# Kernel optimization log

Measured on AMD Instinct MI355X. Metric: run time of the kernel, lower is better.

## Reference

```python
import jax, jax.numpy as jnp
import numpy as np

B, S, D, H = 16, 577, 768, 12  # batch, seq (24*24+1 cls), hidden, heads
WH, WW = 24, 24
HEAD = D // H
NUM_REL = (2 * WH - 1) * (2 * WW - 1) + 3  # 2212


def make_rel_pos_index(wh, ww):
    # mirrors TFData2VecVisionRelativePositionBias.get_position_index
    xx, yy = np.meshgrid(np.arange(wh), np.arange(ww))  # 'xy' indexing like tf.meshgrid
    coords = np.stack([yy, xx], axis=0).reshape(2, -1)  # [2, wh*ww]
    rel = coords[:, :, None] - coords[:, None, :]       # [2, N, N]
    rel = rel.transpose(1, 2, 0)                        # [N, N, 2]
    rx = (rel[:, :, 0] + wh - 1) * (2 * ww - 1)
    ry = rel[:, :, 1] + ww - 1
    idx = rx + ry                                       # [N, N]
    n = idx.shape[0]
    top = np.full((1, n), NUM_REL - 3, dtype=idx.dtype)
    left = np.full((n, 1), NUM_REL - 2, dtype=idx.dtype)
    corner = np.full((1, 1), NUM_REL - 1, dtype=idx.dtype)
    idx = np.concatenate([top, idx], axis=0)
    idx = np.concatenate([np.concatenate([corner, left], axis=0), idx], axis=1)
    return idx.astype(np.int32)  # [N+1, N+1]


def setup_inputs() -> dict:
    key = jax.random.key(0)
    ks = jax.random.split(key, 6)
    scale = 0.02
    return {
        "hidden_states": jax.random.normal(ks[0], (B, S, D), jnp.float32),
        "Wq": jax.random.normal(ks[1], (D, D), jnp.float32) * scale,
        "bq": jnp.zeros((D,), jnp.float32),
        "Wk": jax.random.normal(ks[2], (D, D), jnp.float32) * scale,
        "Wv": jax.random.normal(ks[3], (D, D), jnp.float32) * scale,
        "bv": jnp.zeros((D,), jnp.float32),
        "rel_pos_bias_table": jax.random.normal(ks[4], (NUM_REL, H), jnp.float32) * scale,
        "rel_pos_index": jnp.asarray(make_rel_pos_index(WH, WW)),
    }


def reference(hidden_states, Wq, bq, Wk, Wv, bv, rel_pos_bias_table, rel_pos_index):
    b, s, _ = hidden_states.shape
    q = (hidden_states @ Wq + bq).reshape(b, s, H, HEAD).transpose(0, 2, 1, 3)
    k = (hidden_states @ Wk).reshape(b, s, H, HEAD).transpose(0, 2, 1, 3)
    v = (hidden_states @ Wv + bv).reshape(b, s, H, HEAD).transpose(0, 2, 1, 3)
    scores = jnp.einsum("bhqd,bhkd->bhqk", q, k) / jnp.sqrt(jnp.float32(HEAD))
    # gathered relative position bias: [S, S, H] -> [H, S, S]
    bias = rel_pos_bias_table[rel_pos_index].transpose(2, 0, 1)
    scores = scores + bias[None]
    probs = jax.nn.softmax(scores, axis=-1)
    out = jnp.einsum("bhqk,bhkd->bhqd", probs, v)
    out = out.transpose(0, 2, 1, 3).reshape(b, s, D)
    return out
```

## Files before the change

kernel.cpp:

```cpp
#include <hip/hip_runtime.h>
#include <hip/hip_bf16.h>


typedef __attribute__((ext_vector_type(8))) short bf16x8;
typedef __attribute__((ext_vector_type(4))) float f32x4;
typedef unsigned short u16;

#define SEQ 577
#define MTOT 9232
#define QKV_STRIDE 7090176
#define VT_PITCH 640
#define B_PITCH 640

static __device__ __forceinline__ u16 f2bf(float x) {
  unsigned int u = __float_as_uint(x);
  u = (u + 0x7FFFu + ((u >> 16) & 1u)) >> 16;
  return (u16)u;
}
static __device__ __forceinline__ float bf2f(u16 v) {
  return __uint_as_float(((unsigned int)v) << 16);
}

static __device__ __forceinline__ void gload_lds16(const void* g, void* l) {
  __builtin_amdgcn_global_load_lds(
      (const __attribute__((address_space(1))) unsigned int*)g,
      (__attribute__((address_space(3))) unsigned int*)l, 16, 0, 0);
}

__global__ __launch_bounds__(256) void prep(
    const float* __restrict__ Wq, const float* __restrict__ Wk,
    const float* __restrict__ Wv, const float* __restrict__ X,
    u16* __restrict__ WT, u16* __restrict__ Xb) {
  const int bid = blockIdx.x;
  if (bid < 1728) {
    __shared__ float t[32][33];
    const int z = bid / 576;
    const int rem = bid - z * 576;
    const int kx = rem % 24, ny = rem / 24;
    const float* W = (z == 0) ? Wq : (z == 1) ? Wk : Wv;
    int x = threadIdx.x & 31;
    int y = threadIdx.x >> 5;
    int k0 = kx * 32;
    int n0 = ny * 32;
#pragma unroll
    for (int i = 0; i < 4; ++i)
      t[y + i * 8][x] = W[(size_t)(k0 + y + i * 8) * 768 + n0 + x];
    __syncthreads();
    u16* o = WT + (size_t)z * 589824;
#pragma unroll
    for (int i = 0; i < 4; ++i)
      o[(size_t)(n0 + y + i * 8) * 768 + k0 + x] = f2bf(t[x][y + i * 8]);
  } else {
    size_t i = ((size_t)(bid - 1728) * 256 + threadIdx.x) * 8;
    if (i >= (size_t)MTOT * 768) return;
    const float4* xp = (const float4*)(X + i);
    float4 a = xp[0], b = xp[1];
    u16 pk[8] = {f2bf(a.x), f2bf(a.y), f2bf(a.z), f2bf(a.w),
                 f2bf(b.x), f2bf(b.y), f2bf(b.z), f2bf(b.w)};
    *(int4*)(Xb + i) = *(const int4*)pk;
  }
}

__global__ __launch_bounds__(256) void bias_pre(
    const float* __restrict__ table, const int* __restrict__ idx,
    u16* __restrict__ biasm) {
  int q = blockIdx.x;
  int h = blockIdx.y;
  for (int k = threadIdx.x; k < B_PITCH; k += 256) {
    u16 v = 0;
    if (k < SEQ) v = f2bf(table[idx[q * SEQ + k] * 12 + h]);
    biasm[((size_t)h * SEQ + q) * B_PITCH + k] = v;
  }
}

__global__ __launch_bounds__(256) void transpose_v(
    const u16* __restrict__ v,
    u16* __restrict__ vT) {
  const int tile = blockIdx.x;
  const int bh = blockIdx.y;
  const int b = bh / 12, h = bh % 12;
  const int tid = threadIdx.x;
  __shared__ u16 T[128][64];
  const int s0 = tile * 128;
  const u16* vp = v + (size_t)b * SEQ * 768 + h * 64;
#pragma unroll
  for (int it = 0; it < 4; ++it) {
    int c = tid + it * 256;
    int r = c >> 3, ko = (c & 7) << 3;
    int gs = s0 + r;
    int4 val = make_int4(0, 0, 0, 0);
    if (gs < SEQ) val = *(const int4*)(vp + (size_t)gs * 768 + ko);
    *(int4*)&T[r][ko ^ (((r >> 3) & 7) << 3)] = val;
  }
  __syncthreads();
  u16* op = vT + (size_t)bh * 64 * VT_PITCH;
#pragma unroll
  for (int it = 0; it < 4; ++it) {
    int c = tid + it * 256;
    int d = c >> 4, so = (c & 15) << 3;
    u16 tmp[8];
#pragma unroll
    for (int j = 0; j < 8; ++j) {
      int rr = so + j;
      tmp[j] = T[rr][d ^ (((rr >> 3) & 7) << 3)];
    }
    *(int4*)(op + (size_t)d * VT_PITCH + s0 + so) = *(const int4*)tmp;
  }
}

__global__ __launch_bounds__(256) void qkv_gemm(
    const u16* __restrict__ Xb,
    const u16* __restrict__ WT,
    const float* __restrict__ bq, const float* __restrict__ bv,
    u16* __restrict__ qkv) {
  const int bid = blockIdx.x;
  const int xcd = bid & 7;
  const int local = bid >> 3;
  const int mp = (local / 18) * 8 + xcd;
  if (mp >= 73) return;
  const int nw = local % 18;
  const int widx = nw % 3;
  const int m0 = mp * 128;
  const int n0 = (nw / 3) * 128;

  const int tid = threadIdx.x;
  const int lane = tid & 63;
  const int w = tid >> 6;
  const int wm = (w >> 1) * 64;
  const int wn = (w & 1) * 64;
  const int quad = lane >> 4;
  const int l15 = lane & 15;

  __shared__ u16 SH[2][128][32];

  const u16* Wp = WT + (size_t)widx * 589824;

  const int srow = w * 32 + (lane >> 2);
  const int scol = (lane & 3) * 8;

  f32x4 acc[4][4];
#pragma unroll
  for (int i = 0; i < 4; ++i)
#pragma unroll
    for (int j = 0; j < 4; ++j) acc[i][j] = (f32x4){0.f, 0.f, 0.f, 0.f};

  for (int kt = 0; kt < 24; ++kt) {
    const int k0 = kt * 32;
    {
      int r0 = m0 + srow;
      int r1 = r0 + 16;
      if (r0 > MTOT - 1) r0 = MTOT - 1;
      if (r1 > MTOT - 1) r1 = MTOT - 1;
      gload_lds16(Xb + (size_t)r0 * 768 + k0 + scol, &SH[0][w * 32][0]);
      gload_lds16(Xb + (size_t)r1 * 768 + k0 + scol, &SH[0][w * 32 + 16][0]);
      gload_lds16(Wp + (size_t)(n0 + srow) * 768 + k0 + scol, &SH[1][w * 32][0]);
      gload_lds16(Wp + (size_t)(n0 + srow + 16) * 768 + k0 + scol, &SH[1][w * 32 + 16][0]);
    }
    __syncthreads();
    bf16x8 af[4], bfv[4];
#pragma unroll
    for (int i = 0; i < 4; ++i)
      af[i] = *(const bf16x8*)(&SH[0][wm + i * 16 + l15][quad * 8]);
#pragma unroll
    for (int i = 0; i < 4; ++i)
      bfv[i] = *(const bf16x8*)(&SH[1][wn + i * 16 + l15][quad * 8]);
#pragma unroll
    for (int mt = 0; mt < 4; ++mt)
#pragma unroll
      for (int nt = 0; nt < 4; ++nt)
        acc[mt][nt] = __builtin_amdgcn_mfma_f32_16x16x32_bf16(af[mt], bfv[nt],
                                                              acc[mt][nt], 0, 0, 0);
    __syncthreads();
  }

  const float scale = (widx == 0) ? 0.125f : 1.0f;
  u16* ob = qkv + (size_t)widx * QKV_STRIDE;
  float biasv[4];
#pragma unroll
  for (int nt = 0; nt < 4; ++nt) {
    int n = n0 + wn + nt * 16 + l15;
    biasv[nt] = (widx == 0) ? bq[n] * 0.125f : (widx == 2) ? bv[n] : 0.f;
  }
  u16* S = &SH[0][0][0];
#pragma unroll
  for (int half = 0; half < 2; ++half) {
    if ((w >> 1) == half) {
#pragma unroll
      for (int mt = 0; mt < 4; ++mt)
#pragma unroll
        for (int nt = 0; nt < 4; ++nt)
#pragma unroll
          for (int r = 0; r < 4; ++r) {
            int rowl = mt * 16 + quad * 4 + r;
            int col = wn + nt * 16 + l15;
            int cs = (col + quad * 32) & 127;
            S[rowl * 128 + cs] = f2bf(acc[mt][nt][r] * scale + biasv[nt]);
          }
    }
    __syncthreads();
#pragma unroll
    for (int it = 0; it < 4; ++it) {
      int c = tid + it * 256;
      int rowl = c >> 4, ch = c & 15;
      int m = m0 + half * 64 + rowl;
      if (m < MTOT) {
        int cs = (ch * 8 + ((rowl >> 2) & 3) * 32) & 127;
        *(int4*)(ob + (size_t)m * 768 + n0 + ch * 8) = *(const int4*)&S[rowl * 128 + cs];
      }
    }
    __syncthreads();
  }
}

__global__ __launch_bounds__(512) void attn(
    const u16* __restrict__ qk, const u16* __restrict__ vT,
    const u16* __restrict__ biasm, float* __restrict__ out) {
  const int bh = blockIdx.x;
  const int qt = blockIdx.y;
  const int b = bh / 12, h = bh - b * 12;
  const int tid = threadIdx.x;
  const int lane = tid & 63;
  const int w = tid >> 6;
  const int quad = lane >> 4;
  const int l15 = lane & 15;

  const u16* qp = qk + (size_t)b * SEQ * 768 + h * 64;
  const u16* kp = qp + (size_t)QKV_STRIDE;
  const u16* vtp = vT + (size_t)bh * 64 * VT_PITCH;
  const u16* bp = biasm + (size_t)h * SEQ * B_PITCH;

  __shared__ u16 Ks[64][72];
  __shared__ u16 VTs[64][72];
  __shared__ u16 Ps[8][16][72];

  const int qrow0 = qt * 128 + w * 16;

  bf16x8 qf[2];
  {
    int row = qrow0 + l15;
    if (row > 576) row = 576;
    qf[0] = *(const bf16x8*)(qp + (size_t)row * 768 + quad * 8);
    qf[1] = *(const bf16x8*)(qp + (size_t)row * 768 + 32 + quad * 8);
  }
  int brow[4];
#pragma unroll
  for (int r = 0; r < 4; ++r) {
    int rr = qrow0 + quad * 4 + r;
    if (rr > 576) rr = 576;
    brow[r] = rr;
  }

  float lacc[4] = {0.f, 0.f, 0.f, 0.f};
  f32x4 O[4];
#pragma unroll
  for (int dt = 0; dt < 4; ++dt) O[dt] = (f32x4){0.f, 0.f, 0.f, 0.f};

  for (int kt = 0; kt < 10; ++kt) {
    const int kbase = kt * 64;
    u16 bb[4][4];
#pragma unroll
    for (int nt = 0; nt < 4; ++nt)
#pragma unroll
      for (int r = 0; r < 4; ++r)
        bb[nt][r] = bp[(size_t)brow[r] * B_PITCH + kbase + nt * 16 + l15];

    {
      int rr = tid >> 3, ko = (tid & 7) << 3;
      int gk = kbase + rr;
      int4 kvv = make_int4(0, 0, 0, 0);
      if (gk < SEQ) kvv = *(const int4*)(kp + (size_t)gk * 768 + ko);
      *(int4*)&Ks[rr][ko] = kvv;
      *(int4*)&VTs[rr][ko] = *(const int4*)(vtp + (size_t)rr * VT_PITCH + kbase + ko);
    }
    __syncthreads();

    f32x4 s[4];
#pragma unroll
    for (int nt = 0; nt < 4; ++nt) {
      f32x4 z = (f32x4){bf2f(bb[nt][0]), bf2f(bb[nt][1]),
                        bf2f(bb[nt][2]), bf2f(bb[nt][3])};
      bf16x8 kf0 = *(const bf16x8*)(&Ks[nt * 16 + l15][quad * 8]);
      bf16x8 kf1 = *(const bf16x8*)(&Ks[nt * 16 + l15][32 + quad * 8]);
      z = __builtin_amdgcn_mfma_f32_16x16x32_bf16(qf[0], kf0, z, 0, 0, 0);
      z = __builtin_amdgcn_mfma_f32_16x16x32_bf16(qf[1], kf1, z, 0, 0, 0);
      s[nt] = z;
    }

    const bool full = (kbase + 64 <= SEQ);
#pragma unroll
    for (int nt = 0; nt < 4; ++nt) {
#pragma unroll
      for (int r = 0; r < 4; ++r) {
        float p = __expf(s[nt][r]);
        unsigned int u = __float_as_uint(p);
        float pt = __uint_as_float(u & 0xFFFF0000u);
        if (full) lacc[r] += pt;
        else lacc[r] += ((kbase + nt * 16 + l15) < SEQ) ? pt : 0.f;
        Ps[w][quad * 4 + r][((nt ^ quad) << 4) + l15] = (u16)(u >> 16);
      }
    }

#pragma unroll
    for (int ks = 0; ks < 2; ++ks) {
      int cc = (ks * 32 + quad * 8) ^ ((l15 >> 2) << 4);
      bf16x8 pf = *(const bf16x8*)(&Ps[w][l15][cc]);
#pragma unroll
      for (int dt = 0; dt < 4; ++dt) {
        bf16x8 vf = *(const bf16x8*)(&VTs[dt * 16 + l15][ks * 32 + quad * 8]);
        O[dt] = __builtin_amdgcn_mfma_f32_16x16x32_bf16(pf, vf, O[dt], 0, 0, 0);
      }
    }
    __syncthreads();
  }

#pragma unroll
  for (int r = 0; r < 4; ++r) {
    float l = lacc[r];
    l += __shfl_xor(l, 1);
    l += __shfl_xor(l, 2);
    l += __shfl_xor(l, 4);
    l += __shfl_xor(l, 8);
    int row = qrow0 + quad * 4 + r;
    if (row < SEQ) {
      float inv = 1.f / l;
#pragma unroll
      for (int dt = 0; dt < 4; ++dt)
        out[((size_t)(b * SEQ + row)) * 768 + h * 64 + dt * 16 + l15] = O[dt][r] * inv;
    }
  }
}

extern "C" void kernel_launch(void* const* d_in, const int* in_sizes, int n_in,
                              void* d_out, int out_size, void* d_ws, size_t ws_size,
                              hipStream_t stream) {
  const float* hs = (const float*)d_in[0];
  const float* Wq = (const float*)d_in[1];
  const float* bq = (const float*)d_in[2];
  const float* Wk = (const float*)d_in[3];
  const float* Wv = (const float*)d_in[4];
  const float* bv = (const float*)d_in[5];
  const float* table = (const float*)d_in[6];
  const int* idx = (const int*)d_in[7];
  float* out = (float*)d_out;

  char* ws = (char*)d_ws;
  u16* qkv = (u16*)ws;
  u16* WT = (u16*)(ws + 42541056);
  u16* Xb = (u16*)(ws + 46080000);
  u16* vT = (u16*)(ws + 42541056);
  u16* biasm = (u16*)(ws + 58269696);

  hipLaunchKernelGGL(prep, dim3(5190), dim3(256), 0, stream, Wq, Wk, Wv, hs, WT, Xb);
  hipLaunchKernelGGL(qkv_gemm, dim3(1440), dim3(256), 0, stream, Xb, WT, bq, bv, qkv);
  hipLaunchKernelGGL(bias_pre, dim3(577, 12), dim3(256), 0, stream, table, idx, biasm);
  hipLaunchKernelGGL(transpose_v, dim3(5, 192), dim3(256), 0, stream,
                     qkv + 2 * (size_t)QKV_STRIDE, vT);
  hipLaunchKernelGGL(attn, dim3(192, 5), dim3(512), 0, stream, qkv, vT, biasm, out);
}
```

Before: 214.2 us.

## Double-buffer LDS tiles in QKV GEMM and merge bias/V-transpose kernels

Result: faster. 209.0 us (-2.4%).

```diff
diff --git a/kernel.cpp b/kernel.cpp
--- a/kernel.cpp
+++ b/kernel.cpp
@@ -61,50 +61,52 @@
   }
 }
 
-__global__ __launch_bounds__(256) void bias_pre(
+__global__ __launch_bounds__(256) void prep2(
+    const u16* __restrict__ v,
+    u16* __restrict__ vT,
     const float* __restrict__ table, const int* __restrict__ idx,
     u16* __restrict__ biasm) {
-  int q = blockIdx.x;
-  int h = blockIdx.y;
-  for (int k = threadIdx.x; k < B_PITCH; k += 256) {
-    u16 v = 0;
-    if (k < SEQ) v = f2bf(table[idx[q * SEQ + k] * 12 + h]);
-    biasm[((size_t)h * SEQ + q) * B_PITCH + k] = v;
-  }
-}
-
-__global__ __launch_bounds__(256) void transpose_v(
-    const u16* __restrict__ v,
-    u16* __restrict__ vT) {
-  const int tile = blockIdx.x;
-  const int bh = blockIdx.y;
-  const int b = bh / 12, h = bh % 12;
+  const int bid = blockIdx.x;
   const int tid = threadIdx.x;
-  __shared__ u16 T[128][64];
-  const int s0 = tile * 128;
-  const u16* vp = v + (size_t)b * SEQ * 768 + h * 64;
-#pragma unroll
-  for (int it = 0; it < 4; ++it) {
-    int c = tid + it * 256;
-    int r = c >> 3, ko = (c & 7) << 3;
-    int gs = s0 + r;
-    int4 val = make_int4(0, 0, 0, 0);
-    if (gs < SEQ) val = *(const int4*)(vp + (size_t)gs * 768 + ko);
-    *(int4*)&T[r][ko ^ (((r >> 3) & 7) << 3)] = val;
-  }
-  __syncthreads();
-  u16* op = vT + (size_t)bh * 64 * VT_PITCH;
-#pragma unroll
-  for (int it = 0; it < 4; ++it) {
-    int c = tid + it * 256;
-    int d = c >> 4, so = (c & 15) << 3;
-    u16 tmp[8];
-#pragma unroll
-    for (int j = 0; j < 8; ++j) {
-      int rr = so + j;
-      tmp[j] = T[rr][d ^ (((rr >> 3) & 7) << 3)];
-    }
-    *(int4*)(op + (size_t)d * VT_PITCH + s0 + so) = *(const int4*)tmp;
+  if (bid < 960) {
+    const int tile = bid % 5;
+    const int bh = bid / 5;
+    const int b = bh / 12, h = bh % 12;
+    __shared__ u16 T[128][64];
+    const int s0 = tile * 128;
+    const u16* vp = v + (size_t)b * SEQ * 768 + h * 64;
+#pragma unroll
+    for (int it = 0; it < 4; ++it) {
+      int c = tid + it * 256;
+      int r = c >> 3, ko = (c & 7) << 3;
+      int gs = s0 + r;
+      int4 val = make_int4(0, 0, 0, 0);
+      if (gs < SEQ) val = *(const int4*)(vp + (size_t)gs * 768 + ko);
+      *(int4*)&T[r][ko ^ (((r >> 3) & 7) << 3)] = val;
+    }
+    __syncthreads();
+    u16* op = vT + (size_t)bh * 64 * VT_PITCH;
+#pragma unroll
+    for (int it = 0; it < 4; ++it) {
+      int c = tid + it * 256;
+      int d = c >> 4, so = (c & 15) << 3;
+      u16 tmp[8];
+#pragma unroll
+      for (int j = 0; j < 8; ++j) {
+        int rr = so + j;
+        tmp[j] = T[rr][d ^ (((rr >> 3) & 7) << 3)];
+      }
+      *(int4*)(op + (size_t)d * VT_PITCH + s0 + so) = *(const int4*)tmp;
+    }
+  } else {
+    const int r = bid - 960;
+    const int q = r % 577;
+    const int h = r / 577;
+    for (int k = tid; k < B_PITCH; k += 256) {
+      u16 vv = 0;
+      if (k < SEQ) vv = f2bf(table[idx[q * SEQ + k] * 12 + h]);
+      biasm[((size_t)h * SEQ + q) * B_PITCH + k] = vv;
+    }
   }
 }
 
@@ -131,39 +133,51 @@
   const int quad = lane >> 4;
   const int l15 = lane & 15;
 
-  __shared__ u16 SH[2][128][32];
+  __shared__ u16 SH[2][2][128][32];
 
   const u16* Wp = WT + (size_t)widx * 589824;
 
   const int srow = w * 32 + (lane >> 2);
   const int scol = (lane & 3) * 8;
 
+  int r0 = m0 + srow;
+  int r1 = r0 + 16;
+  if (r0 > MTOT - 1) r0 = MTOT - 1;
+  if (r1 > MTOT - 1) r1 = MTOT - 1;
+  const u16* a0 = Xb + (size_t)r0 * 768 + scol;
+  const u16* a1 = Xb + (size_t)r1 * 768 + scol;
+  const u16* b0 = Wp + (size_t)(n0 + srow) * 768 + scol;
+  const u16* b1 = Wp + (size_t)(n0 + srow + 16) * 768 + scol;
+
   f32x4 acc[4][4];
 #pragma unroll
   for (int i = 0; i < 4; ++i)
 #pragma unroll
     for (int j = 0; j < 4; ++j) acc[i][j] = (f32x4){0.f, 0.f, 0.f, 0.f};
 
+  gload_lds16(a0, &SH[0][0][w * 32][0]);
+  gload_lds16(a1, &SH[0][0][w * 32 + 16][0]);
+  gload_lds16(b0, &SH[0][1][w * 32][0]);
+  gload_lds16(b1, &SH[0][1][w * 32 + 16][0]);
+  __syncthreads();
+
   for (int kt = 0; kt < 24; ++kt) {
-    const int k0 = kt * 32;
-    {
-      int r0 = m0 + srow;
-      int r1 = r0 + 16;
-      if (r0 > MTOT - 1) r0 = MTOT - 1;
-      if (r1 > MTOT - 1) r1 = MTOT - 1;
-      gload_lds16(Xb + (size_t)r0 * 768 + k0 + scol, &SH[0][w * 32][0]);
-      gload_lds16(Xb + (size_t)r1 * 768 + k0 + scol, &SH[0][w * 32 + 16][0]);
-      gload_lds16(Wp + (size_t)(n0 + srow) * 768 + k0 + scol, &SH[1][w * 32][0]);
-      gload_lds16(Wp + (size_t)(n0 + srow + 16) * 768 + k0 + scol, &SH[1][w * 32 + 16][0]);
-    }
-    __syncthreads();
+    const int cur = kt & 1;
+    if (kt < 23) {
+      const int k1 = (kt + 1) * 32;
+      const int nb = cur ^ 1;
+      gload_lds16(a0 + k1, &SH[nb][0][w * 32][0]);
+      gload_lds16(a1 + k1, &SH[nb][0][w * 32 + 16][0]);
+      gload_lds16(b0 + k1, &SH[nb][1][w * 32][0]);
+      gload_lds16(b1 + k1, &SH[nb][1][w * 32 + 16][0]);
+    }
     bf16x8 af[4], bfv[4];
 #pragma unroll
     for (int i = 0; i < 4; ++i)
-      af[i] = *(const bf16x8*)(&SH[0][wm + i * 16 + l15][quad * 8]);
+      af[i] = *(const bf16x8*)(&SH[cur][0][wm + i * 16 + l15][quad * 8]);
 #pragma unroll
     for (int i = 0; i < 4; ++i)
-      bfv[i] = *(const bf16x8*)(&SH[1][wn + i * 16 + l15][quad * 8]);
+      bfv[i] = *(const bf16x8*)(&SH[cur][1][wn + i * 16 + l15][quad * 8]);
 #pragma unroll
     for (int mt = 0; mt < 4; ++mt)
 #pragma unroll
@@ -181,7 +195,7 @@
     int n = n0 + wn + nt * 16 + l15;
     biasv[nt] = (widx == 0) ? bq[n] * 0.125f : (widx == 2) ? bv[n] : 0.f;
   }
-  u16* S = &SH[0][0][0];
+  u16* S = &SH[0][0][0][0];
 #pragma unroll
   for (int half = 0; half < 2; ++half) {
     if ((w >> 1) == half) {
@@ -352,8 +366,7 @@
 
   hipLaunchKernelGGL(prep, dim3(5190), dim3(256), 0, stream, Wq, Wk, Wv, hs, WT, Xb);
   hipLaunchKernelGGL(qkv_gemm, dim3(1440), dim3(256), 0, stream, Xb, WT, bq, bv, qkv);
-  hipLaunchKernelGGL(bias_pre, dim3(577, 12), dim3(256), 0, stream, table, idx, biasm);
-  hipLaunchKernelGGL(transpose_v, dim3(5, 192), dim3(256), 0, stream,
-                     qkv + 2 * (size_t)QKV_STRIDE, vT);
+  hipLaunchKernelGGL(prep2, dim3(7884), dim3(256), 0, stream,
+                     qkv + 2 * (size_t)QKV_STRIDE, vT, table, idx, biasm);
   hipLaunchKernelGGL(attn, dim3(192, 5), dim3(512), 0, stream, qkv, vT, biasm, out);
 }
```
